# Performance work log

Hardware: AMD Instinct MI355X
Metric: run time of the kernel (lower is better)

The kernel has to match this reference:

```python
import jax, jax.numpy as jnp
import numpy as np

B, Q, C = 2, 1568, 768
H = 12
FN, S = 8, 196


def setup_inputs() -> dict:
    key = jax.random.key(0)
    ks = jax.random.split(key, 8)
    init = lambda k, shape: jax.random.normal(k, shape, jnp.float32) * 0.02
    return {
        "query": jax.random.normal(ks[0], (B, Q, C), jnp.float32),
        "memory": jax.random.normal(ks[1], (B, FN * S, C), jnp.float32),
        "Wq": init(ks[2], (C, C)),
        "Wkv": init(ks[3], (C, 2 * C)),
        "Wpq": init(ks[4], (C, C)),
        "Wpkv": init(ks[5], (C, 2 * C)),
        "Wproj": init(ks[6], (C, C)),
        "bproj": jnp.zeros((C,), jnp.float32),
        "seq_len": S,
        "num_frames": FN,
    }


def reference(query, memory, Wq, Wkv, Wpq, Wpkv, Wproj, bproj, seq_len, num_frames):
    Bn, N, Cn = memory.shape
    h = H
    d = Cn // h
    Fn, Sn = num_frames, seq_len
    Qn = query.shape[1]
    scale = d ** -0.5

    # stage 1: per-frame spatial attention
    q = query @ Wq                                   # [B,Q,C]
    k, v = jnp.split(memory @ Wkv, 2, axis=-1)       # [B,N,C] each
    qh = q.reshape(Bn, Qn, h, d)
    kh = k.reshape(Bn, Fn, Sn, h, d)
    vh = v.reshape(Bn, Fn, Sn, h, d)
    space_attn = scale * jnp.einsum('bqhd,bfshd->bhqfs', qh, kh)  # [B,h,Q,F,S]
    attn = jax.nn.softmax(space_attn, axis=-1)        # softmax over tokens within each frame
    # per-frame summaries: [B,Q,F,C]
    x = jnp.einsum('bhqfs,bfshd->bqfhd', attn, vh).reshape(Bn, Qn, Fn, Cn)

    # stage 2: temporal attention over frame summaries
    k2, v2 = jnp.split(x @ Wpkv, 2, axis=-1)
    k2 = k2.reshape(Bn, Qn, Fn, h, d).transpose(0, 3, 1, 2, 4)   # [B,h,Q,F,d]
    v2 = v2.reshape(Bn, Qn, Fn, h, d).transpose(0, 3, 1, 2, 4)   # [B,h,Q,F,d]
    q2 = (q @ Wpq).reshape(Bn, Qn, h, d).transpose(0, 2, 1, 3) * scale  # [B,h,Q,d]
    attn2 = jax.nn.softmax(jnp.einsum('bhqd,bhqfd->bhqf', q2, k2), axis=-1)
    # faithful to source einsum 'b h q f, b h s f d -> b h q d': v2's query axis is summed out
    q_out = jnp.einsum('bhqf,bhsfd->bhqd', attn2, v2)             # [B,h,Q,d]
    q_out = q_out.transpose(0, 2, 1, 3).reshape(Bn, Qn, Cn) @ Wproj + bproj

    # source returns pre-softmax scaled scores with shape (B*h, Q, F, S)
    return q_out, space_attn.reshape(Bn * h, Qn, Fn, Sn)
```

## Files before the change

### kernel.cpp

```cpp
#include <hip/hip_runtime.h>

#define B_   2
#define Q_   1568
#define C_   768
#define C2_  1536
#define H_   12
#define D_   64
#define F_   8
#define S_   196
#define N_   1568
constexpr float SCALE = 0.125f;

typedef __bf16 bf16_t;
typedef __bf16 bf16x8 __attribute__((ext_vector_type(8)));
typedef __bf16 bf16x4 __attribute__((ext_vector_type(4)));
typedef float  f32x4  __attribute__((ext_vector_type(4)));

#define AS_G __attribute__((address_space(1)))
#define AS_L __attribute__((address_space(3)))

__device__ inline void load_lds16(const void* g, void* l) {
    __builtin_amdgcn_global_load_lds((const AS_G unsigned int*)g,
                                     (AS_L unsigned int*)l, 16, 0, 0);
}

#define CVT_N1 602112
#define CVT_N2 1204224
#define CVT_N3 1499136
__global__ __launch_bounds__(256) void cvt3(
    const float* __restrict__ q, const float* __restrict__ mem,
    const float* __restrict__ wpkv,
    bf16_t* __restrict__ qo, bf16_t* __restrict__ mo, bf16_t* __restrict__ wo)
{
    int i = blockIdx.x * 256 + threadIdx.x;
    const float* src; bf16_t* dst; int off;
    if (i < CVT_N1)      { src = q;    dst = qo; off = i; }
    else if (i < CVT_N2) { src = mem;  dst = mo; off = i - CVT_N1; }
    else if (i < CVT_N3) { src = wpkv; dst = wo; off = i - CVT_N2; }
    else return;
    float4 v = ((const float4*)src)[off];
    bf16x4 o = { (bf16_t)v.x, (bf16_t)v.y, (bf16_t)v.z, (bf16_t)v.w };
    ((bf16x4*)dst)[off] = o;
}

__global__ __launch_bounds__(256) void transpose4(
    const float* __restrict__ W0, const float* __restrict__ W1,
    const float* __restrict__ W2, const float* __restrict__ W3,
    bf16_t* __restrict__ T0, bf16_t* __restrict__ T1,
    bf16_t* __restrict__ T2, bf16_t* __restrict__ T3)
{
    const int zi = blockIdx.z;
    const float* W = (zi == 0) ? W0 : (zi == 1) ? W1 : (zi == 2) ? W2 : W3;
    bf16_t* Wt     = (zi == 0) ? T0 : (zi == 1) ? T1 : (zi == 2) ? T2 : T3;
    const int N = (zi == 1) ? C2_ : C_;
    const int K = C_;
    const int n0 = blockIdx.x * 32;
    if (n0 >= N) return;
    __shared__ float tile[32][33];
    const int k0 = blockIdx.y * 32;
    const int t = threadIdx.x;
    const int tx = t & 31, ty = t >> 5;
#pragma unroll
    for (int i = 0; i < 4; i++)
        tile[ty + i * 8][tx] = W[(size_t)(k0 + ty + i * 8) * N + n0 + tx];
    __syncthreads();
#pragma unroll
    for (int i = 0; i < 4; i++)
        Wt[(size_t)(n0 + ty + i * 8) * K + k0 + tx] = (bf16_t)tile[tx][ty + i * 8];
}

__global__ __launch_bounds__(256) void gemm_mfma(
    const bf16_t* __restrict__ A, const bf16_t* __restrict__ Bt,
    float* __restrict__ C, bf16_t* __restrict__ Cbf,
    int M, int N, int K, const float* __restrict__ bias)
{
    __shared__ bf16_t As[2][128 * 32];
    __shared__ bf16_t Bs[2][128 * 32];
    const int n0 = blockIdx.x * 128;
    const int m0 = blockIdx.y * 128;
    const int t = threadIdx.x;
    const int lane = t & 63;
    const int wv = t >> 6;
    const int wm = wv >> 1, wn = wv & 1;
    const int lane15 = lane & 15, quad = lane >> 4;

    f32x4 acc[4][4];
#pragma unroll
    for (int i = 0; i < 4; i++)
#pragma unroll
        for (int j = 0; j < 4; j++) acc[i][j] = (f32x4){0.f, 0.f, 0.f, 0.f};

    const int row0 = t >> 2,          kc0 = (t & 3) ^ (row0 & 3);
    const int row1 = (256 + t) >> 2,  kc1 = (t & 3) ^ (row1 & 3);
    int rg0 = m0 + row0; if (rg0 >= M) rg0 = M - 1;
    int rg1 = m0 + row1; if (rg1 >= M) rg1 = M - 1;
    const bf16_t* a0 = A  + (size_t)rg0 * K + kc0 * 8;
    const bf16_t* a1 = A  + (size_t)rg1 * K + kc1 * 8;
    const bf16_t* b0 = Bt + (size_t)(n0 + row0) * K + kc0 * 8;
    const bf16_t* b1 = Bt + (size_t)(n0 + row1) * K + kc1 * 8;
    const int dst0 = (0 * 256 + wv * 64) * 16;
    const int dst1 = (1 * 256 + wv * 64) * 16;

    auto stage = [&](int buf, int k0) {
        load_lds16(a0 + k0, (char*)As[buf] + dst0);
        load_lds16(b0 + k0, (char*)Bs[buf] + dst0);
        load_lds16(a1 + k0, (char*)As[buf] + dst1);
        load_lds16(b1 + k0, (char*)Bs[buf] + dst1);
    };

    stage(0, 0);
    __syncthreads();
    int cur = 0;
    const int posA = quad ^ (lane15 & 3);
    for (int k0 = 0; k0 < K; k0 += 32) {
        if (k0 + 32 < K) stage(cur ^ 1, k0 + 32);

        const bf16_t* Ab = As[cur];
        const bf16_t* Bb = Bs[cur];
        bf16x8 af[4], bfr[4];
#pragma unroll
        for (int i = 0; i < 4; i++) {
            af[i]  = *(const bf16x8*)(Ab + (wm * 64 + i * 16 + lane15) * 32 + posA * 8);
            bfr[i] = *(const bf16x8*)(Bb + (wn * 64 + i * 16 + lane15) * 32 + posA * 8);
        }
#pragma unroll
        for (int i = 0; i < 4; i++)
#pragma unroll
            for (int j = 0; j < 4; j++)
                acc[i][j] = __builtin_amdgcn_mfma_f32_16x16x32_bf16(af[i], bfr[j], acc[i][j], 0, 0, 0);

        __syncthreads();
        cur ^= 1;
    }

#pragma unroll
    for (int i = 0; i < 4; i++) {
#pragma unroll
        for (int j = 0; j < 4; j++) {
            int col = n0 + wn * 64 + j * 16 + lane15;
            float bb = bias ? bias[col] : 0.f;
#pragma unroll
            for (int r = 0; r < 4; r++) {
                int row = m0 + wm * 64 + i * 16 + quad * 4 + r;
                if (row < M) {
                    float v = acc[i][j][r] + bb;
                    if (C)   C[(size_t)row * N + col] = v;
                    if (Cbf) Cbf[(size_t)row * N + col] = (bf16_t)v;
                }
            }
        }
    }
}

__global__ __launch_bounds__(256) void gemm_g(
    const bf16_t* __restrict__ q2b, const bf16_t* __restrict__ wkvb,
    bf16_t* __restrict__ G, int M)
{
    __shared__ bf16_t As[128 * 64];
    __shared__ bf16_t Bs[128 * 64];
    const int n0 = blockIdx.x * 128;
    const int m0 = blockIdx.y * 128;
    const int h  = blockIdx.z;
    const int t = threadIdx.x;
    const int lane = t & 63, wv = t >> 6;
    const int wm = wv >> 1, wn = wv & 1;
    const int lane15 = lane & 15, quad = lane >> 4;

#pragma unroll
    for (int i = 0; i < 4; i++) {
        int c = i * 256 + t;
        int row = c >> 3, kc = (c & 7) ^ (row & 7);
        int rg = m0 + row; if (rg >= M) rg = M - 1;
        load_lds16(q2b + (size_t)rg * C_ + h * 64 + kc * 8,
                   (char*)As + (i * 256 + wv * 64) * 16);
        load_lds16(wkvb + (size_t)(n0 + row) * C2_ + h * 64 + kc * 8,
                   (char*)Bs + (i * 256 + wv * 64) * 16);
    }
    __syncthreads();

    f32x4 acc[4][4];
#pragma unroll
    for (int i = 0; i < 4; i++)
#pragma unroll
        for (int j = 0; j < 4; j++) acc[i][j] = (f32x4){0.f, 0.f, 0.f, 0.f};

    bf16x8 af[4][2], bfr[4][2];
#pragma unroll
    for (int i = 0; i < 4; i++)
#pragma unroll
        for (int kk = 0; kk < 2; kk++) {
            int rowa = wm * 64 + i * 16 + lane15;
            int rowb = wn * 64 + i * 16 + lane15;
            int pos = (kk * 4 + quad) ^ (lane15 & 7);
            af[i][kk]  = *(const bf16x8*)(As + rowa * 64 + pos * 8);
            bfr[i][kk] = *(const bf16x8*)(Bs + rowb * 64 + pos * 8);
        }
#pragma unroll
    for (int i = 0; i < 4; i++)
#pragma unroll
        for (int j = 0; j < 4; j++)
#pragma unroll
            for (int kk = 0; kk < 2; kk++)
                acc[i][j] = __builtin_amdgcn_mfma_f32_16x16x32_bf16(af[i][kk], bfr[j][kk], acc[i][j], 0, 0, 0);

#pragma unroll
    for (int i = 0; i < 4; i++)
#pragma unroll
        for (int j = 0; j < 4; j++) {
            int col = n0 + wn * 64 + j * 16 + lane15;
#pragma unroll
            for (int r = 0; r < 4; r++) {
                int row = m0 + wm * 64 + i * 16 + quad * 4 + r;
                if (row < M)
                    G[(size_t)row * (H_ * C_) + h * C_ + col] = (bf16_t)acc[i][j][r];
            }
        }
}

__global__ __launch_bounds__(256) void l2_kernel(
    const bf16_t* __restrict__ x, const bf16_t* __restrict__ G,
    float* __restrict__ l2out)
{
    __shared__ bf16_t xs[F_ * C_];
    __shared__ bf16_t gs[H_ * C_];
    const int bq = blockIdx.x;
    const int t = threadIdx.x;
    const bf16x8* xsrc = (const bf16x8*)(x + (size_t)bq * F_ * C_);
    for (int e = t; e < F_ * C_ / 8; e += 256) ((bf16x8*)xs)[e] = xsrc[e];
    const bf16x8* gsrc = (const bf16x8*)(G + (size_t)bq * H_ * C_);
    for (int e = t; e < H_ * C_ / 8; e += 256) ((bf16x8*)gs)[e] = gsrc[e];
    __syncthreads();
    if (t < 96) {
        int h = t >> 3, f = t & 7;
        float acc = 0.f;
        for (int c = 0; c < C_; c += 8) {
            bf16x8 xv = *(const bf16x8*)(xs + f * C_ + c);
            bf16x8 gv = *(const bf16x8*)(gs + h * C_ + c);
#pragma unroll
            for (int j = 0; j < 8; j++) acc += (float)xv[j] * (float)gv[j];
        }
        l2out[(size_t)bq * 96 + t] = SCALE * acc;
    }
}

__global__ __launch_bounds__(448, 4) void attn1_fused(
    const bf16_t* __restrict__ qb, const bf16_t* __restrict__ kvb,
    float* __restrict__ out1, bf16_t* __restrict__ x, float* __restrict__ xsum)
{
    __shared__ bf16_t Vt[64 * 232];
    __shared__ bf16_t Ps[7 * 16 * 232];
    const int f = blockIdx.x, qt = blockIdx.y, z = blockIdx.z;
    const int b = z / H_, h = z - b * H_;
    const int t = threadIdx.x;
    const int lane = t & 63, w = t >> 6;
    const int lane15 = lane & 15, quad = lane >> 4;

    const size_t kvBase = ((size_t)b * N_ + (size_t)f * S_) * C2_;

    bf16x8 vreg[4];
#pragma unroll
    for (int i = 0; i < 4; i++) {
        int e = t + 448 * i;
        int dg = e / S_, s = e - dg * S_;
        if (e >= 8 * S_) { dg = 0; s = 0; }
        vreg[i] = *(const bf16x8*)(kvb + kvBase + (size_t)s * C2_ + C_ + h * D_ + dg * 8);
    }

    const int qrow = qt * 112 + w * 16 + lane15;
    const bf16_t* qp = qb + ((size_t)b * Q_ + qrow) * C_ + h * D_ + quad * 8;
    bf16x8 qa0 = *(const bf16x8*)(qp);
    bf16x8 qa1 = *(const bf16x8*)(qp + 32);

#pragma unroll
    for (int i = 0; i < 4; i++) {
        int e = t + 448 * i;
        if (e < 64 * 28) {
            int dd = e / 28;
            int s  = S_ + (e - dd * 28);
            Vt[dd * 232 + s] = (bf16_t)0.f;
        }
    }
    bf16_t* Pw = Ps + w * (16 * 232);
    {
        int prow = lane >> 2, c0 = 208 + (lane & 3) * 4;
        *(bf16x4*)(Pw + prow * 232 + c0) =
            (bf16x4){(bf16_t)0.f, (bf16_t)0.f, (bf16_t)0.f, (bf16_t)0.f};
    }

    f32x4 acc[13];
#pragma unroll
    for (int n = 0; n < 13; n++) acc[n] = (f32x4){0.f, 0.f, 0.f, 0.f};
#pragma unroll
    for (int n = 0; n < 13; n++) {
        int srow = n * 16 + lane15; if (srow > S_ - 1) srow = S_ - 1;
        const bf16_t* kp = kvb + kvBase + (size_t)srow * C2_ + h * D_ + quad * 8;
        bf16x8 kb0 = *(const bf16x8*)(kp);
        bf16x8 kb1 = *(const bf16x8*)(kp + 32);
        acc[n] = __builtin_amdgcn_mfma_f32_16x16x32_bf16(qa0, kb0, acc[n], 0, 0, 0);
        acc[n] = __builtin_amdgcn_mfma_f32_16x16x32_bf16(qa1, kb1, acc[n], 0, 0, 0);
    }

    const size_t o1base = ((size_t)z * Q_ + qt * 112 + w * 16 + quad * 4) * N_ + (size_t)f * S_;
#pragma unroll
    for (int n = 0; n < 13; n++) {
        int s = n * 16 + lane15;
        bool valid = s < S_;
#pragma unroll
        for (int r = 0; r < 4; r++) {
            float v = SCALE * acc[n][r];
            if (valid) out1[o1base + (size_t)r * N_ + s] = v;
            acc[n][r] = valid ? v : -3e38f;
        }
    }

    float m[4], inv[4];
#pragma unroll
    for (int r = 0; r < 4; r++) {
        float mm = acc[0][r];
#pragma unroll
        for (int n = 1; n < 13; n++) mm = fmaxf(mm, acc[n][r]);
        mm = fmaxf(mm, __shfl_xor(mm, 1));
        mm = fmaxf(mm, __shfl_xor(mm, 2));
        mm = fmaxf(mm, __shfl_xor(mm, 4));
        mm = fmaxf(mm, __shfl_xor(mm, 8));
        m[r] = mm;
    }
#pragma unroll
    for (int r = 0; r < 4; r++) {
        float ss = 0.f;
#pragma unroll
        for (int n = 0; n < 13; n++) {
            float e = __expf(acc[n][r] - m[r]);
            acc[n][r] = e;
            ss += e;
        }
        ss += __shfl_xor(ss, 1);
        ss += __shfl_xor(ss, 2);
        ss += __shfl_xor(ss, 4);
        ss += __shfl_xor(ss, 8);
        inv[r] = 1.f / ss;
    }

#pragma unroll
    for (int i = 0; i < 4; i++) {
        int e = t + 448 * i;
        if (e < 8 * S_) {
            int dg = e / S_, s = e - dg * S_;
#pragma unroll
            for (int j = 0; j < 8; j++)
                Vt[(dg * 8 + j) * 232 + s] = vreg[i][j];
        }
    }

#pragma unroll
    for (int n = 0; n < 13; n++)
#pragma unroll
        for (int r = 0; r < 4; r++)
            Pw[(quad * 4 + r) * 232 + n * 16 + lane15] = (bf16_t)(acc[n][r] * inv[r]);

    __syncthreads();

    bf16x8 pa[7];
#pragma unroll
    for (int ks = 0; ks < 7; ks++)
        pa[ks] = *(const bf16x8*)(Pw + lane15 * 232 + ks * 32 + quad * 8);

    f32x4 o[4];
#pragma unroll
    for (int nt = 0; nt < 4; nt++) o[nt] = (f32x4){0.f, 0.f, 0.f, 0.f};
#pragma unroll
    for (int nt = 0; nt < 4; nt++)
#pragma unroll
        for (int ks = 0; ks < 7; ks++) {
            bf16x8 vb = *(const bf16x8*)(Vt + (nt * 16 + lane15) * 232 + ks * 32 + quad * 8);
            o[nt] = __builtin_amdgcn_mfma_f32_16x16x32_bf16(pa[ks], vb, o[nt], 0, 0, 0);
        }

    const int qb2 = qt * 112 + w * 16 + quad * 4;
#pragma unroll
    for (int nt = 0; nt < 4; nt++)
#pragma unroll
        for (int r = 0; r < 4; r++)
            x[(((size_t)(b * Q_ + qb2 + r)) * F_ + f) * C_ + h * D_ + nt * 16 + lane15] =
                (bf16_t)o[nt][r];

    float part[4];
#pragma unroll
    for (int nt = 0; nt < 4; nt++)
        part[nt] = o[nt][0] + o[nt][1] + o[nt][2] + o[nt][3];
    __syncthreads();
    float* red = (float*)Vt;
    if (t < 64) red[t] = 0.f;
    __syncthreads();
#pragma unroll
    for (int nt = 0; nt < 4; nt++)
        atomicAdd(&red[nt * 16 + lane15], part[nt]);
    __syncthreads();
    if (t < 64)
        atomicAdd(&xsum[((size_t)(b * F_ + f)) * C_ + h * D_ + t], red[t]);
}

__global__ __launch_bounds__(256) void vsum_kernel(
    const float* __restrict__ xsum, const float* __restrict__ Wpkv,
    float* __restrict__ vsum)
{
    __shared__ float xs[C_];
    const int bf = blockIdx.x;
    const int t = threadIdx.x;
    for (int i = 0; i < 3; i++) xs[t + 256 * i] = xsum[(size_t)bf * C_ + t + 256 * i];
    __syncthreads();
    const int c2 = blockIdx.y * 256 + t;
    float acc = 0.f;
#pragma unroll 8
    for (int c = 0; c < C_; c++) acc += xs[c] * Wpkv[(size_t)c * C2_ + C_ + c2];
    vsum[(size_t)bf * C_ + c2] = acc;
}

__global__ __launch_bounds__(256) void attn2_qout(
    const float* __restrict__ logits2, const float* __restrict__ vsum,
    bf16_t* __restrict__ qout)
{
    __shared__ float p2s[96];
    const int bq = blockIdx.x;
    const int t = threadIdx.x;

    if (t < 96) {
        float l = logits2[(size_t)bq * 96 + t];
        float mm = l;
        mm = fmaxf(mm, __shfl_xor(mm, 1));
        mm = fmaxf(mm, __shfl_xor(mm, 2));
        mm = fmaxf(mm, __shfl_xor(mm, 4));
        float e = __expf(l - mm);
        float ss = e;
        ss += __shfl_xor(ss, 1);
        ss += __shfl_xor(ss, 2);
        ss += __shfl_xor(ss, 4);
        p2s[t] = e / ss;
    }
    __syncthreads();

    const int b = bq / Q_;
    for (int i = 0; i < 3; i++) {
        int c = t + 256 * i;
        int h = c >> 6;
        float acc = 0.f;
#pragma unroll
        for (int fr = 0; fr < F_; fr++)
            acc += p2s[h * 8 + fr] * vsum[((size_t)(b * F_ + fr)) * C_ + c];
        qout[(size_t)bq * C_ + c] = (bf16_t)acc;
    }
}

extern "C" void kernel_launch(void* const* d_in, const int* in_sizes, int n_in,
                              void* d_out, int out_size, void* d_ws, size_t ws_size,
                              hipStream_t stream) {
    const float* query  = (const float*)d_in[0];
    const float* memory = (const float*)d_in[1];
    const float* Wq     = (const float*)d_in[2];
    const float* Wkv    = (const float*)d_in[3];
    const float* Wpq    = (const float*)d_in[4];
    const float* Wpkv   = (const float*)d_in[5];
    const float* Wproj  = (const float*)d_in[6];
    const float* bproj  = (const float*)d_in[7];

    float* out0 = (float*)d_out;
    float* out1 = (float*)d_out + (size_t)B_ * Q_ * C_;

    char* w = (char*)d_ws;
    bf16_t* kv_bf = (bf16_t*)(w + 0);
    bf16_t* q_bf  = (bf16_t*)(w + 9633792);
    bf16_t* q2b   = (bf16_t*)(w + 14450688);
    bf16_t* qry_b = (bf16_t*)(w + 19267584);
    bf16_t* mem_b = (bf16_t*)(w + 24084480);
    bf16_t* qo_bf = (bf16_t*)(w + 28901376);
    bf16_t* x_bf  = (bf16_t*)(w + 33718272);
    bf16_t* G_bf  = (bf16_t*)(w + 72253440);
    float*  lgt2  = (float*) (w + 130056192);
    bf16_t* Wqt   = (bf16_t*)(w + 131260416);
    bf16_t* Wkvt  = (bf16_t*)(w + 132440064);
    bf16_t* Wpqt  = (bf16_t*)(w + 134799360);
    bf16_t* Wprjt = (bf16_t*)(w + 135979008);
    bf16_t* Wpkvb = (bf16_t*)(w + 137158656);
    float*  xsum  = (float*) (w + 139517952);
    float*  vsum  = (float*) (w + 139567104);

    const int MQ = B_ * Q_;
    const int MN = B_ * N_;

    cvt3<<<5856, 256, 0, stream>>>(query, memory, Wpkv, qry_b, mem_b, Wpkvb);
    transpose4<<<dim3(48, 24, 4), 256, 0, stream>>>(Wq, Wkv, Wpq, Wproj,
                                                    Wqt, Wkvt, Wpqt, Wprjt);

    gemm_mfma<<<dim3(6, 25), 256, 0, stream>>>(qry_b, Wqt, nullptr, q_bf, MQ, C_, C_, nullptr);
    gemm_mfma<<<dim3(12, 25), 256, 0, stream>>>(mem_b, Wkvt, nullptr, kv_bf, MN, C2_, C_, nullptr);
    gemm_mfma<<<dim3(6, 25), 256, 0, stream>>>(q_bf, Wpqt, nullptr, q2b, MQ, C_, C_, nullptr);
    hipMemsetAsync(xsum, 0, (size_t)B_ * F_ * C_ * sizeof(float), stream);
    attn1_fused<<<dim3(F_, 14, B_ * H_), 448, 0, stream>>>(q_bf, kv_bf, out1, x_bf, xsum);
    gemm_g<<<dim3(6, 25, H_), 256, 0, stream>>>(q2b, Wpkvb, G_bf, MQ);
    l2_kernel<<<MQ, 256, 0, stream>>>(x_bf, G_bf, lgt2);
    vsum_kernel<<<dim3(16, 3), 256, 0, stream>>>(xsum, Wpkv, vsum);
    attn2_qout<<<MQ, 256, 0, stream>>>(lgt2, vsum, qo_bf);
    gemm_mfma<<<dim3(6, 25), 256, 0, stream>>>(qo_bf, Wprjt, out0, nullptr, MQ, C_, C_, bproj);
}
```

Measured before the change: 623.0 us.

## Merge Q/KV projection GEMMs, use MFMA for temporal logits, retile spatial attention

```diff
diff --git a/kernel.cpp b/kernel.cpp
--- a/kernel.cpp
+++ b/kernel.cpp
@@ -69,15 +69,14 @@
         Wt[(size_t)(n0 + ty + i * 8) * K + k0 + tx] = (bf16_t)tile[tx][ty + i * 8];
 }
 
-__global__ __launch_bounds__(256) void gemm_mfma(
+__device__ inline void gemm_body(
     const bf16_t* __restrict__ A, const bf16_t* __restrict__ Bt,
     float* __restrict__ C, bf16_t* __restrict__ Cbf,
-    int M, int N, int K, const float* __restrict__ bias)
-{
-    __shared__ bf16_t As[2][128 * 32];
-    __shared__ bf16_t Bs[2][128 * 32];
-    const int n0 = blockIdx.x * 128;
-    const int m0 = blockIdx.y * 128;
+    int M, int N, int K, const float* __restrict__ bias,
+    int bx, int by, bf16_t* As, bf16_t* Bs)
+{
+    const int n0 = bx * 128;
+    const int m0 = by * 128;
     const int t = threadIdx.x;
     const int lane = t & 63;
     const int wv = t >> 6;
@@ -102,10 +101,10 @@
     const int dst1 = (1 * 256 + wv * 64) * 16;
 
     auto stage = [&](int buf, int k0) {
-        load_lds16(a0 + k0, (char*)As[buf] + dst0);
-        load_lds16(b0 + k0, (char*)Bs[buf] + dst0);
-        load_lds16(a1 + k0, (char*)As[buf] + dst1);
-        load_lds16(b1 + k0, (char*)Bs[buf] + dst1);
+        load_lds16(a0 + k0, (char*)(As + buf * 128 * 32) + dst0);
+        load_lds16(b0 + k0, (char*)(Bs + buf * 128 * 32) + dst0);
+        load_lds16(a1 + k0, (char*)(As + buf * 128 * 32) + dst1);
+        load_lds16(b1 + k0, (char*)(Bs + buf * 128 * 32) + dst1);
     };
 
     stage(0, 0);
@@ -115,8 +114,8 @@
     for (int k0 = 0; k0 < K; k0 += 32) {
         if (k0 + 32 < K) stage(cur ^ 1, k0 + 32);
 
-        const bf16_t* Ab = As[cur];
-        const bf16_t* Bb = Bs[cur];
+        const bf16_t* Ab = As + cur * 128 * 32;
+        const bf16_t* Bb = Bs + cur * 128 * 32;
         bf16x8 af[4], bfr[4];
 #pragma unroll
         for (int i = 0; i < 4; i++) {
@@ -152,6 +151,30 @@
     }
 }
 
+__global__ __launch_bounds__(256) void gemm_mfma(
+    const bf16_t* __restrict__ A, const bf16_t* __restrict__ Bt,
+    float* __restrict__ C, bf16_t* __restrict__ Cbf,
+    int M, int N, int K, const float* __restrict__ bias)
+{
+    __shared__ bf16_t As[2 * 128 * 32];
+    __shared__ bf16_t Bs[2 * 128 * 32];
+    gemm_body(A, Bt, C, Cbf, M, N, K, bias, blockIdx.x, blockIdx.y, As, Bs);
+}
+
+__global__ __launch_bounds__(256) void gemm_qkv(
+    const bf16_t* __restrict__ qry, const bf16_t* __restrict__ Wqt,
+    bf16_t* __restrict__ qo,
+    const bf16_t* __restrict__ mem, const bf16_t* __restrict__ Wkvt,
+    bf16_t* __restrict__ kvo)
+{
+    __shared__ bf16_t As[2 * 128 * 32];
+    __shared__ bf16_t Bs[2 * 128 * 32];
+    if (blockIdx.x < 6)
+        gemm_body(qry, Wqt, nullptr, qo,  B_ * Q_, C_,  C_, nullptr, blockIdx.x,     blockIdx.y, As, Bs);
+    else
+        gemm_body(mem, Wkvt, nullptr, kvo, B_ * N_, C2_, C_, nullptr, blockIdx.x - 6, blockIdx.y, As, Bs);
+}
+
 __global__ __launch_bounds__(256) void gemm_g(
     const bf16_t* __restrict__ q2b, const bf16_t* __restrict__ wkvb,
     bf16_t* __restrict__ G, int M)
@@ -217,38 +240,44 @@
         }
 }
 
-__global__ __launch_bounds__(256) void l2_kernel(
+__global__ __launch_bounds__(256) void l2_mfma(
     const bf16_t* __restrict__ x, const bf16_t* __restrict__ G,
     float* __restrict__ l2out)
 {
-    __shared__ bf16_t xs[F_ * C_];
-    __shared__ bf16_t gs[H_ * C_];
-    const int bq = blockIdx.x;
-    const int t = threadIdx.x;
-    const bf16x8* xsrc = (const bf16x8*)(x + (size_t)bq * F_ * C_);
-    for (int e = t; e < F_ * C_ / 8; e += 256) ((bf16x8*)xs)[e] = xsrc[e];
-    const bf16x8* gsrc = (const bf16x8*)(G + (size_t)bq * H_ * C_);
-    for (int e = t; e < H_ * C_ / 8; e += 256) ((bf16x8*)gs)[e] = gsrc[e];
-    __syncthreads();
-    if (t < 96) {
-        int h = t >> 3, f = t & 7;
-        float acc = 0.f;
-        for (int c = 0; c < C_; c += 8) {
-            bf16x8 xv = *(const bf16x8*)(xs + f * C_ + c);
-            bf16x8 gv = *(const bf16x8*)(gs + h * C_ + c);
-#pragma unroll
-            for (int j = 0; j < 8; j++) acc += (float)xv[j] * (float)gv[j];
-        }
-        l2out[(size_t)bq * 96 + t] = SCALE * acc;
-    }
-}
-
-__global__ __launch_bounds__(448, 4) void attn1_fused(
+    const int t = threadIdx.x;
+    const int lane = t & 63, w = t >> 6;
+    const int lane15 = lane & 15, quad = lane >> 4;
+    const int bq = blockIdx.x * 4 + w;
+    const int fr = lane15 < F_ ? lane15 : F_ - 1;
+    const int hr = lane15 < H_ ? lane15 : H_ - 1;
+    const bf16_t* xa = x + ((size_t)bq * F_ + fr) * C_ + quad * 8;
+    const bf16_t* gb = G + ((size_t)bq * H_ + hr) * C_ + quad * 8;
+
+    f32x4 acc0 = (f32x4){0.f, 0.f, 0.f, 0.f};
+    f32x4 acc1 = (f32x4){0.f, 0.f, 0.f, 0.f};
+#pragma unroll 4
+    for (int c = 0; c < C_; c += 64) {
+        bf16x8 a0 = *(const bf16x8*)(xa + c);
+        bf16x8 b0 = *(const bf16x8*)(gb + c);
+        bf16x8 a1 = *(const bf16x8*)(xa + c + 32);
+        bf16x8 b1 = *(const bf16x8*)(gb + c + 32);
+        acc0 = __builtin_amdgcn_mfma_f32_16x16x32_bf16(a0, b0, acc0, 0, 0, 0);
+        acc1 = __builtin_amdgcn_mfma_f32_16x16x32_bf16(a1, b1, acc1, 0, 0, 0);
+    }
+#pragma unroll
+    for (int r = 0; r < 4; r++) {
+        int ff = quad * 4 + r;
+        if (ff < F_ && lane15 < H_)
+            l2out[(size_t)bq * 96 + lane15 * 8 + ff] = SCALE * (acc0[r] + acc1[r]);
+    }
+}
+
+__global__ __launch_bounds__(256, 2) void attn1_fused(
     const bf16_t* __restrict__ qb, const bf16_t* __restrict__ kvb,
     float* __restrict__ out1, bf16_t* __restrict__ x, float* __restrict__ xsum)
 {
     __shared__ bf16_t Vt[64 * 232];
-    __shared__ bf16_t Ps[7 * 16 * 232];
+    __shared__ bf16_t Ps[4 * 16 * 232];
     const int f = blockIdx.x, qt = blockIdx.y, z = blockIdx.z;
     const int b = z / H_, h = z - b * H_;
     const int t = threadIdx.x;
@@ -257,23 +286,24 @@
 
     const size_t kvBase = ((size_t)b * N_ + (size_t)f * S_) * C2_;
 
-    bf16x8 vreg[4];
-#pragma unroll
-    for (int i = 0; i < 4; i++) {
-        int e = t + 448 * i;
+    bf16x8 vreg[7];
+#pragma unroll
+    for (int i = 0; i < 7; i++) {
+        int e = t + 256 * i;
         int dg = e / S_, s = e - dg * S_;
         if (e >= 8 * S_) { dg = 0; s = 0; }
         vreg[i] = *(const bf16x8*)(kvb + kvBase + (size_t)s * C2_ + C_ + h * D_ + dg * 8);
     }
 
-    const int qrow = qt * 112 + w * 16 + lane15;
-    const bf16_t* qp = qb + ((size_t)b * Q_ + qrow) * C_ + h * D_ + quad * 8;
+    const int qrow = qt * 64 + w * 16 + lane15;
+    const int qrc = qrow < Q_ ? qrow : Q_ - 1;
+    const bf16_t* qp = qb + ((size_t)b * Q_ + qrc) * C_ + h * D_ + quad * 8;
     bf16x8 qa0 = *(const bf16x8*)(qp);
     bf16x8 qa1 = *(const bf16x8*)(qp + 32);
 
 #pragma unroll
-    for (int i = 0; i < 4; i++) {
-        int e = t + 448 * i;
+    for (int i = 0; i < 7; i++) {
+        int e = t + 256 * i;
         if (e < 64 * 28) {
             int dd = e / 28;
             int s  = S_ + (e - dd * 28);
@@ -300,7 +330,8 @@
         acc[n] = __builtin_amdgcn_mfma_f32_16x16x32_bf16(qa1, kb1, acc[n], 0, 0, 0);
     }
 
-    const size_t o1base = ((size_t)z * Q_ + qt * 112 + w * 16 + quad * 4) * N_ + (size_t)f * S_;
+    const int qbase = qt * 64 + w * 16 + quad * 4;
+    const size_t o1base = ((size_t)z * Q_ + qbase) * N_ + (size_t)f * S_;
 #pragma unroll
     for (int n = 0; n < 13; n++) {
         int s = n * 16 + lane15;
@@ -308,7 +339,7 @@
 #pragma unroll
         for (int r = 0; r < 4; r++) {
             float v = SCALE * acc[n][r];
-            if (valid) out1[o1base + (size_t)r * N_ + s] = v;
+            if (valid && (qbase + r) < Q_) out1[o1base + (size_t)r * N_ + s] = v;
             acc[n][r] = valid ? v : -3e38f;
         }
     }
@@ -342,8 +373,8 @@
     }
 
 #pragma unroll
-    for (int i = 0; i < 4; i++) {
-        int e = t + 448 * i;
+    for (int i = 0; i < 7; i++) {
+        int e = t + 256 * i;
         if (e < 8 * S_) {
             int dg = e / S_, s = e - dg * S_;
 #pragma unroll
@@ -376,18 +407,22 @@
             o[nt] = __builtin_amdgcn_mfma_f32_16x16x32_bf16(pa[ks], vb, o[nt], 0, 0, 0);
         }
 
-    const int qb2 = qt * 112 + w * 16 + quad * 4;
 #pragma unroll
     for (int nt = 0; nt < 4; nt++)
 #pragma unroll
         for (int r = 0; r < 4; r++)
-            x[(((size_t)(b * Q_ + qb2 + r)) * F_ + f) * C_ + h * D_ + nt * 16 + lane15] =
-                (bf16_t)o[nt][r];
+            if (qbase + r < Q_)
+                x[(((size_t)(b * Q_ + qbase + r)) * F_ + f) * C_ + h * D_ + nt * 16 + lane15] =
+                    (bf16_t)o[nt][r];
 
     float part[4];
 #pragma unroll
-    for (int nt = 0; nt < 4; nt++)
-        part[nt] = o[nt][0] + o[nt][1] + o[nt][2] + o[nt][3];
+    for (int nt = 0; nt < 4; nt++) {
+        part[nt] = 0.f;
+#pragma unroll
+        for (int r = 0; r < 4; r++)
+            if (qbase + r < Q_) part[nt] += o[nt][r];
+    }
     __syncthreads();
     float* red = (float*)Vt;
     if (t < 64) red[t] = 0.f;
@@ -485,19 +520,17 @@
     float*  vsum  = (float*) (w + 139567104);
 
     const int MQ = B_ * Q_;
-    const int MN = B_ * N_;
 
     cvt3<<<5856, 256, 0, stream>>>(query, memory, Wpkv, qry_b, mem_b, Wpkvb);
     transpose4<<<dim3(48, 24, 4), 256, 0, stream>>>(Wq, Wkv, Wpq, Wproj,
                                                     Wqt, Wkvt, Wpqt, Wprjt);
 
-    gemm_mfma<<<dim3(6, 25), 256, 0, stream>>>(qry_b, Wqt, nullptr, q_bf, MQ, C_, C_, nullptr);
-    gemm_mfma<<<dim3(12, 25), 256, 0, stream>>>(mem_b, Wkvt, nullptr, kv_bf, MN, C2_, C_, nullptr);
+    gemm_qkv<<<dim3(18, 25), 256, 0, stream>>>(qry_b, Wqt, q_bf, mem_b, Wkvt, kv_bf);
     gemm_mfma<<<dim3(6, 25), 256, 0, stream>>>(q_bf, Wpqt, nullptr, q2b, MQ, C_, C_, nullptr);
     hipMemsetAsync(xsum, 0, (size_t)B_ * F_ * C_ * sizeof(float), stream);
-    attn1_fused<<<dim3(F_, 14, B_ * H_), 448, 0, stream>>>(q_bf, kv_bf, out1, x_bf, xsum);
+    attn1_fused<<<dim3(F_, 25, B_ * H_), 256, 0, stream>>>(q_bf, kv_bf, out1, x_bf, xsum);
     gemm_g<<<dim3(6, 25, H_), 256, 0, stream>>>(q2b, Wpkvb, G_bf, MQ);
-    l2_kernel<<<MQ, 256, 0, stream>>>(x_bf, G_bf, lgt2);
+    l2_mfma<<<MQ / 4, 256, 0, stream>>>(x_bf, G_bf, lgt2);
     vsum_kernel<<<dim3(16, 3), 256, 0, stream>>>(xsum, Wpkv, vsum);
     attn2_qout<<<MQ, 256, 0, stream>>>(lgt2, vsum, qo_bf);
     gemm_mfma<<<dim3(6, 25), 256, 0, stream>>>(qo_bf, Wprjt, out0, nullptr, MQ, C_, C_, bproj);
```

Result: faster. 572.3 us (-8.1%).
